# Kernel optimization log

Measured on AMD Instinct MI355X. Metric: run time of the kernel, lower is better.

## Reference

```python
import jax, jax.numpy as jnp
import numpy as np

# dims: B=4 batch, S=512 seq, P=128 input_size, C=64 classes(=hidden_size), K=64 gln layer width, 4 context bits -> 16 contexts
B, S, P, C, K, NBITS = 4, 512, 128, 64, 64, 4
NCTX = 2 ** NBITS
LOGIT_CLIP = 5.0


def setup_inputs() -> dict:
    key = jax.random.key(0)
    ks = jax.random.split(key, 8)
    return {
        "x": jax.random.normal(ks[0], (B, S, P), jnp.float32),
        "hidden": jax.random.normal(ks[1], (B, C), jnp.float32),
        # GLN layer 1: per-class, per-neuron halfspace context hyperplanes and gated weights
        "H1": jax.random.normal(ks[2], (C, K, NBITS, P), jnp.float32),
        "W1": jax.random.normal(ks[3], (C, K, NCTX, P), jnp.float32) / np.sqrt(P),
        # GLN output layer: one neuron per class
        "H2": jax.random.normal(ks[4], (C, NBITS, P), jnp.float32),
        "W2": jax.random.normal(ks[5], (C, NCTX, K), jnp.float32) / np.sqrt(K),
        # fc2: Linear(input_size, hidden_size)
        "fc2_w": jax.random.normal(ks[6], (C, P), jnp.float32) / np.sqrt(P),
        "fc2_b": jnp.zeros((C,), jnp.float32),
    }


def _ctx_index(bits):
    # bits: (..., NBITS) bool -> integer context id in [0, 2^NBITS)
    return (bits * (2 ** jnp.arange(NBITS, dtype=jnp.int32))).sum(-1)


def _gln_predict(x, H1, W1, H2, W2):
    # base predictions: sigmoid(x) -> logit space is x itself (clipped for stability)
    l0 = jnp.clip(x, -LOGIT_CLIP, LOGIT_CLIP)  # (B,S,P)
    # layer 1: halfspace gating then geometric mixing in logit space
    ctx1 = _ctx_index(jnp.einsum('bsp,ckjp->bsckj', x, H1) > 0)          # (B,S,C,K)
    mix1 = jnp.einsum('bsp,ckxp->bsckx', l0, W1)                          # (B,S,C,K,NCTX)
    l1 = jnp.take_along_axis(mix1, ctx1[..., None], axis=-1)[..., 0]      # (B,S,C,K)
    l1 = jnp.clip(l1, -LOGIT_CLIP, LOGIT_CLIP)
    # output layer: one gated neuron per class
    ctx2 = _ctx_index(jnp.einsum('bsp,cjp->bscj', x, H2) > 0)             # (B,S,C)
    mix2 = jnp.einsum('bsck,cxk->bscx', l1, W2)                           # (B,S,C,NCTX)
    l2 = jnp.take_along_axis(mix2, ctx2[..., None], axis=-1)[..., 0]      # (B,S,C)
    return jax.nn.sigmoid(l2)


def reference(x, hidden, H1, W1, H2, W2, fc2_w, fc2_b):
    b = _gln_predict(x, H1, W1, H2, W2)                   # (B,S,C)
    # multihead gating
    sig_alphas = jax.nn.sigmoid(x @ fc2_w.T + fc2_b)      # (B,S,C)
    b = b * sig_alphas

    # sequential roll+add+relu recurrence over seq_len
    def step(h, bt):
        h = jax.nn.relu(bt + jnp.roll(h, 1, axis=-1))
        return h, h

    h_last, outs = jax.lax.scan(step, hidden, jnp.swapaxes(b, 0, 1))  # outs: (S,B,C)
    outputs = jnp.swapaxes(outs, 0, 1)                                # (B,S,C)
    return outputs, h_last
```

## Files before the change

kernel.cpp:

```cpp
#include <hip/hip_runtime.h>
#include <math.h>

#define BB 4
#define SS 512
#define PP 128
#define CC 64
#define KK 64
#define NCTX_ 16
#define TT 64
#define NTILES ((BB*SS)/TT)

typedef __attribute__((ext_vector_type(8))) short bf16x8;
typedef __attribute__((ext_vector_type(4))) float f32x4;
typedef __attribute__((ext_vector_type(16))) float f32x16;

static __device__ __forceinline__ float bf2f(short h) {
    unsigned u = ((unsigned)(unsigned short)h) << 16;
    return __builtin_bit_cast(float, u);
}
static __device__ __forceinline__ short f2bf(float f) {
    unsigned u = __builtin_bit_cast(unsigned, f);
    unsigned r = (u + 0x7fffu + ((u >> 16) & 1u)) >> 16;
    return (short)(unsigned short)r;
}
static __device__ __forceinline__ bf16x8 clampfrag(bf16x8 h) {
    typedef __attribute__((ext_vector_type(4))) unsigned u32x4;
    u32x4 u = __builtin_bit_cast(u32x4, h);
    #pragma unroll
    for (int i = 0; i < 4; ++i) {
        const unsigned w = u[i];
        const unsigned s = w & 0x80008000u;
        unsigned lo = w & 0x7fffu;
        unsigned hi = (w >> 16) & 0x7fffu;
        lo = lo > 0x40a0u ? 0x40a0u : lo;
        hi = hi > 0x40a0u ? 0x40a0u : hi;
        u[i] = s | lo | (hi << 16);
    }
    return __builtin_bit_cast(bf16x8, u);
}

__global__ __launch_bounds__(256) void pack_kernel(
    const float* __restrict__ W1, const float* __restrict__ H1,
    const float* __restrict__ H2, const float* __restrict__ fc2w,
    short* __restrict__ W1h, short* __restrict__ H1h32, short* __restrict__ H1l32,
    short* __restrict__ H2Wh, short* __restrict__ H2Wl)
{
    const int bid  = blockIdx.x;
    const int w    = threadIdx.x >> 6;
    const int lane = threadIdx.x & 63;

    if (bid < CC * KK) {
        const int tile = bid;
        const int q    = w;
        const float4* src = reinterpret_cast<const float4*>(
            W1 + ((size_t)tile * 16 + (lane >> 2)) * PP + q * 32 + (lane & 3) * 8);
        const float4 v0 = src[0], v1 = src[1];
        const float vv[8] = {v0.x, v0.y, v0.z, v0.w, v1.x, v1.y, v1.z, v1.w};
        bf16x8 hh;
        #pragma unroll
        for (int e = 0; e < 8; ++e) hh[e] = f2bf(vv[e]);
        const int lp = (lane & 3) * 16 + (lane >> 2);
        *reinterpret_cast<bf16x8*>(W1h + (((size_t)tile * 4 + q) * 64 + lp) * 8) = hh;
    } else if (bid < CC * KK + 1024) {
        const int gw  = (bid - CC * KK) * 4 + w;
        const int row = (gw >> 3) * 32 + (lane & 31);
        const int col = (gw & 7) * 16 + (lane >> 5) * 8;
        const float4* s = reinterpret_cast<const float4*>(H1 + (size_t)row * PP + col);
        const float4 a = s[0], b = s[1];
        const float vv[8] = {a.x, a.y, a.z, a.w, b.x, b.y, b.z, b.w};
        bf16x8 hh, ll;
        #pragma unroll
        for (int e = 0; e < 8; ++e) {
            const short hv = f2bf(vv[e]);
            hh[e] = hv;
            ll[e] = f2bf(vv[e] - bf2f(hv));
        }
        const size_t o = ((size_t)gw * 64 + lane) * 8;
        *reinterpret_cast<bf16x8*>(H1h32 + o) = hh;
        *reinterpret_cast<bf16x8*>(H1l32 + o) = ll;
    } else {
        const int cidx = bid - (CC * KK + 1024);
        #pragma unroll
        for (int i = 0; i < 2; ++i) {
            const int q8  = w * 2 + i;
            const int row = lane & 31;
            const int col = q8 * 16 + (lane >> 5) * 8;
            float vv[8];
            if (row < 4) {
                const float4* s = reinterpret_cast<const float4*>(
                    H2 + ((size_t)cidx * 4 + row) * PP + col);
                const float4 a = s[0], b = s[1];
                vv[0]=a.x; vv[1]=a.y; vv[2]=a.z; vv[3]=a.w;
                vv[4]=b.x; vv[5]=b.y; vv[6]=b.z; vv[7]=b.w;
            } else if (row == 4) {
                const float4* s = reinterpret_cast<const float4*>(
                    fc2w + (size_t)cidx * PP + col);
                const float4 a = s[0], b = s[1];
                vv[0]=a.x; vv[1]=a.y; vv[2]=a.z; vv[3]=a.w;
                vv[4]=b.x; vv[5]=b.y; vv[6]=b.z; vv[7]=b.w;
            } else {
                #pragma unroll
                for (int e = 0; e < 8; ++e) vv[e] = 0.f;
            }
            bf16x8 hh, ll;
            #pragma unroll
            for (int e = 0; e < 8; ++e) {
                const short hv = f2bf(vv[e]);
                hh[e] = hv;
                ll[e] = f2bf(vv[e] - bf2f(hv));
            }
            const size_t o = (((size_t)cidx * 8 + q8) * 64 + lane) * 8;
            *reinterpret_cast<bf16x8*>(H2Wh + o) = hh;
            *reinterpret_cast<bf16x8*>(H2Wl + o) = ll;
        }
    }
}

__global__ __launch_bounds__(256, 4) void predict_kernel(
    const float* __restrict__ x,
    const short* __restrict__ H1h32,
    const short* __restrict__ H1l32,
    const short* __restrict__ W1h,
    const short* __restrict__ H2Wh,
    const short* __restrict__ H2Wl,
    const float* __restrict__ W2,
    const float* __restrict__ fc2b,
    float* __restrict__ bout)
{
    __shared__ short xuh[2][8][64][8];
    __shared__ short xul[2][8][64][8];
    __shared__ unsigned char ctxb[TT][68];
    __shared__ unsigned char bit2b[TT];
    __shared__ float af[TT];

    const int tid  = threadIdx.x;
    const int lane = tid & 63;
    const int wid  = __builtin_amdgcn_readfirstlane(tid >> 6);
    const int bid  = blockIdx.x;
    const int sw   = ((bid & 7) << 8) | (bid >> 3);
    const int c    = sw >> 5;
    const int tile = sw & (NTILES - 1);
    const int tok0 = tile * TT;

    const int t15 = lane & 15;
    const int g   = lane >> 4;
    const int l31 = lane & 31;
    const int l5  = lane >> 5;
    const f32x4  zero4  = {0.f, 0.f, 0.f, 0.f};
    const f32x16 zero16 = {0.f,0.f,0.f,0.f,0.f,0.f,0.f,0.f,
                           0.f,0.f,0.f,0.f,0.f,0.f,0.f,0.f};

    {
        const int tok = tid >> 2;
        const int qq  = tid & 3;
        const int ct  = tok >> 5;
        const float4* x4 = reinterpret_cast<const float4*>(
            x + (size_t)(tok0 + tok) * PP + qq * 32);
        float v[32];
        #pragma unroll
        for (int i = 0; i < 8; ++i) {
            const float4 t = x4[i];
            v[i*4+0]=t.x; v[i*4+1]=t.y; v[i*4+2]=t.z; v[i*4+3]=t.w;
        }
        #pragma unroll
        for (int gg = 0; gg < 4; ++gg) {
            const int q8 = qq * 2 + (gg >> 1);
            const int lw = (gg & 1) * 32 + (tok & 31);
            bf16x8 hh, ll;
            #pragma unroll
            for (int e = 0; e < 8; ++e) {
                const float f = v[gg*8+e];
                const short hv = f2bf(f);
                hh[e] = hv;
                ll[e] = f2bf(f - bf2f(hv));
            }
            *reinterpret_cast<bf16x8*>(&xuh[ct][q8][lw][0]) = hh;
            *reinterpret_cast<bf16x8*>(&xul[ct][q8][lw][0]) = ll;
        }
    }
    __syncthreads();

    #pragma unroll
    for (int rt = 0; rt < 2; ++rt) {
        f32x16 aA = zero16, aB = zero16;
        const size_t tb = ((size_t)(c * 8 + wid * 2 + rt)) * 8;
        #pragma unroll
        for (int q8 = 0; q8 < 8; ++q8) {
            const size_t fo = ((tb + q8) * 64 + lane) * 8;
            const bf16x8 ah  = *reinterpret_cast<const bf16x8*>(H1h32 + fo);
            const bf16x8 al  = *reinterpret_cast<const bf16x8*>(H1l32 + fo);
            const bf16x8 bh0 = *reinterpret_cast<const bf16x8*>(&xuh[0][q8][lane][0]);
            const bf16x8 bl0 = *reinterpret_cast<const bf16x8*>(&xul[0][q8][lane][0]);
            const bf16x8 bh1 = *reinterpret_cast<const bf16x8*>(&xuh[1][q8][lane][0]);
            const bf16x8 bl1 = *reinterpret_cast<const bf16x8*>(&xul[1][q8][lane][0]);
            aA = __builtin_amdgcn_mfma_f32_32x32x16_bf16(ah, bh0, aA, 0, 0, 0);
            aA = __builtin_amdgcn_mfma_f32_32x32x16_bf16(ah, bl0, aA, 0, 0, 0);
            aA = __builtin_amdgcn_mfma_f32_32x32x16_bf16(al, bh0, aA, 0, 0, 0);
            aB = __builtin_amdgcn_mfma_f32_32x32x16_bf16(ah, bh1, aB, 0, 0, 0);
            aB = __builtin_amdgcn_mfma_f32_32x32x16_bf16(ah, bl1, aB, 0, 0, 0);
            aB = __builtin_amdgcn_mfma_f32_32x32x16_bf16(al, bh1, aB, 0, 0, 0);
        }
        #pragma unroll
        for (int rg = 0; rg < 4; ++rg) {
            const int k = wid * 16 + rt * 8 + 2 * rg + l5;
            const int cvA = (aA[4*rg+0] > 0.f ? 1 : 0) | (aA[4*rg+1] > 0.f ? 2 : 0) |
                            (aA[4*rg+2] > 0.f ? 4 : 0) | (aA[4*rg+3] > 0.f ? 8 : 0);
            const int cvB = (aB[4*rg+0] > 0.f ? 1 : 0) | (aB[4*rg+1] > 0.f ? 2 : 0) |
                            (aB[4*rg+2] > 0.f ? 4 : 0) | (aB[4*rg+3] > 0.f ? 8 : 0);
            ctxb[l31][k]      = (unsigned char)cvA;
            ctxb[32 + l31][k] = (unsigned char)cvB;
        }
    }

    if (wid < 2) {
        f32x16 a2 = zero16;
        #pragma unroll
        for (int q8 = 0; q8 < 8; ++q8) {
            const size_t fo = (((size_t)c * 8 + q8) * 64 + lane) * 8;
            const bf16x8 ah = *reinterpret_cast<const bf16x8*>(H2Wh + fo);
            const bf16x8 al = *reinterpret_cast<const bf16x8*>(H2Wl + fo);
            const bf16x8 bh = *reinterpret_cast<const bf16x8*>(&xuh[wid][q8][lane][0]);
            const bf16x8 bl = *reinterpret_cast<const bf16x8*>(&xul[wid][q8][lane][0]);
            a2 = __builtin_amdgcn_mfma_f32_32x32x16_bf16(ah, bh, a2, 0, 0, 0);
            a2 = __builtin_amdgcn_mfma_f32_32x32x16_bf16(ah, bl, a2, 0, 0, 0);
            a2 = __builtin_amdgcn_mfma_f32_32x32x16_bf16(al, bh, a2, 0, 0, 0);
        }
        const int tok = wid * 32 + l31;
        if (l5 == 0) {
            bit2b[tok] = (unsigned char)((a2[0] > 0.f ? 1 : 0) | (a2[1] > 0.f ? 2 : 0) |
                                         (a2[2] > 0.f ? 4 : 0) | (a2[3] > 0.f ? 8 : 0));
        } else {
            af[tok] = a2[0];
        }
    }
    __syncthreads();

    short* l1s = &xul[0][0][0][0];
    {
        bf16x8 ch[4][4];
        #pragma unroll
        for (int j = 0; j < 4; ++j)
            #pragma unroll
            for (int q = 0; q < 4; ++q) {
                const int q8 = 2 * q + (g >> 1);
                const int lw = (g & 1) * 32 + (j & 1) * 16 + t15;
                ch[j][q] = clampfrag(*reinterpret_cast<const bf16x8*>(&xuh[j >> 1][q8][lw][0]));
            }

        #pragma unroll 4
        for (int k16 = 0; k16 < 16; ++k16) {
            const int k = wid * 16 + k16;
            f32x4 acc[4] = {zero4, zero4, zero4, zero4};
            #pragma unroll
            for (int q = 0; q < 4; ++q) {
                const size_t fo = (((size_t)(c * KK + k) * 4 + q) * 64 + lane) * 8;
                const bf16x8 ah = *reinterpret_cast<const bf16x8*>(W1h + fo);
                #pragma unroll
                for (int j = 0; j < 4; ++j)
                    acc[j] = __builtin_amdgcn_mfma_f32_16x16x32_bf16(ah, ch[j][q], acc[j], 0, 0, 0);
            }
            #pragma unroll
            for (int j = 0; j < 4; ++j) {
                const int tok = j * 16 + t15;
                const int cx  = ctxb[tok][k];
                const int sel = cx & 3;
                const float v = (sel == 0) ? acc[j][0] : (sel == 1) ? acc[j][1] :
                                (sel == 2) ? acc[j][2] : acc[j][3];
                if (g == (cx >> 2))
                    l1s[tok * 68 + k] = f2bf(fminf(fmaxf(v, -5.f), 5.f));
            }
        }
    }
    __syncthreads();

    {
        const int tok = tid >> 2;
        const int qt  = tid & 3;
        const int ctx2 = bit2b[tok];
        const float4* w2p = reinterpret_cast<const float4*>(
            W2 + ((size_t)c * NCTX_ + ctx2) * KK + qt * 16);
        float s = 0.f;
        #pragma unroll
        for (int i4 = 0; i4 < 4; ++i4) {
            const float4 w = w2p[i4];
            const int kb = tok * 68 + qt * 16 + i4 * 4;
            s = fmaf(w.x, bf2f(l1s[kb + 0]),
                fmaf(w.y, bf2f(l1s[kb + 1]),
                fmaf(w.z, bf2f(l1s[kb + 2]),
                fmaf(w.w, bf2f(l1s[kb + 3]), s))));
        }
        s += __shfl_xor(s, 1, 64);
        s += __shfl_xor(s, 2, 64);
        if (qt == 0) {
            const float alpha = af[tok] + fc2b[c];
            const float bv = (1.f / (1.f + expf(-s))) * (1.f / (1.f + expf(-alpha)));
            bout[(size_t)(tok0 + tok) * CC + c] = bv;
        }
    }
}

__global__ __launch_bounds__(256, 4) void predict_fb_kernel(
    const float* __restrict__ x,
    const float* __restrict__ H1,
    const float* __restrict__ W1b,
    const float* __restrict__ H2,
    const float* __restrict__ W2,
    const float* __restrict__ fc2w,
    const float* __restrict__ fc2b,
    float* __restrict__ bout)
{
    __shared__ float xs[PP][TT + 1];
    __shared__ float bitss[4][TT];
    __shared__ float apart[4][TT];
    __shared__ float l2part[4][TT];

    const int tid  = threadIdx.x;
    const int lane = tid & 63;
    const int wid  = __builtin_amdgcn_readfirstlane(tid >> 6);
    const int bid  = blockIdx.x;
    const int sw   = ((bid & 7) << 8) | (bid >> 3);
    const int c    = sw >> 5;
    const int tile = sw & (NTILES - 1);
    const int tok0 = tile * TT;

    {
        const float4* xg = reinterpret_cast<const float4*>(x + (size_t)tok0 * PP);
        #pragma unroll
        for (int it = 0; it < (TT * PP / 4) / 256; ++it) {
            const int i = it * 256 + tid;
            const float4 v = xg[i];
            const int t = i >> 5;
            const int p = (i & 31) << 2;
            xs[p + 0][t] = v.x; xs[p + 1][t] = v.y;
            xs[p + 2][t] = v.z; xs[p + 3][t] = v.w;
        }
    }
    __syncthreads();

    int ctxreg[16];
    {
        const float4* H1c4 = reinterpret_cast<const float4*>(H1 + (size_t)c * KK * 4 * PP);
        #pragma unroll
        for (int gg = 0; gg < 8; ++gg) {
            const int k = wid * 16 + gg * 2;
            const float4* h4 = H1c4 + (size_t)k * 4 * 32;
            float acc[8] = {0.f, 0.f, 0.f, 0.f, 0.f, 0.f, 0.f, 0.f};
            #pragma unroll 2
            for (int p4 = 0; p4 < 32; ++p4) {
                const float x0 = xs[4 * p4 + 0][lane];
                const float x1 = xs[4 * p4 + 1][lane];
                const float x2 = xs[4 * p4 + 2][lane];
                const float x3 = xs[4 * p4 + 3][lane];
                #pragma unroll
                for (int r = 0; r < 8; ++r) {
                    const float4 w = h4[r * 32 + p4];
                    acc[r] = fmaf(w.w, x3, fmaf(w.z, x2, fmaf(w.y, x1, fmaf(w.x, x0, acc[r]))));
                }
            }
            ctxreg[gg * 2]     = (acc[0] > 0.f ? 1 : 0) | (acc[1] > 0.f ? 2 : 0) |
                                 (acc[2] > 0.f ? 4 : 0) | (acc[3] > 0.f ? 8 : 0);
            ctxreg[gg * 2 + 1] = (acc[4] > 0.f ? 1 : 0) | (acc[5] > 0.f ? 2 : 0) |
                                 (acc[6] > 0.f ? 4 : 0) | (acc[7] > 0.f ? 8 : 0);
        }
    }
    {
        const float4* h2 = reinterpret_cast<const float4*>(H2 + ((size_t)c * 4 + wid) * PP);
        float d = 0.f;
        #pragma unroll 8
        for (int p4 = 0; p4 < 32; ++p4) {
            const float4 w = h2[p4];
            d = fmaf(w.w, xs[4 * p4 + 3][lane], fmaf(w.z, xs[4 * p4 + 2][lane],
                fmaf(w.y, xs[4 * p4 + 1][lane], fmaf(w.x, xs[4 * p4 + 0][lane], d))));
        }
        bitss[wid][lane] = (d > 0.f) ? 1.f : 0.f;
        const float4* fw = reinterpret_cast<const float4*>(fc2w + (size_t)c * PP) + wid * 8;
        float ap = 0.f;
        #pragma unroll
        for (int p4 = 0; p4 < 8; ++p4) {
            const float4 w = fw[p4];
            const int p = wid * 32 + 4 * p4;
            ap = fmaf(w.w, xs[p + 3][lane], fmaf(w.z, xs[p + 2][lane],
                 fmaf(w.y, xs[p + 1][lane], fmaf(w.x, xs[p + 0][lane], ap))));
        }
        apart[wid][lane] = ap;
    }
    __syncthreads();

    float l1v[16];
    {
        const float4* W1c4 = reinterpret_cast<const float4*>(W1b) +
                             (size_t)(c * KK + wid * 16) * 512;
        #pragma unroll
        for (int gg = 0; gg < 2; ++gg) {
            float s[8] = {0.f, 0.f, 0.f, 0.f, 0.f, 0.f, 0.f, 0.f};
            const float4* wp[8];
            #pragma unroll
            for (int jj = 0; jj < 8; ++jj) {
                const int kk = gg * 8 + jj;
                wp[jj] = W1c4 + (size_t)kk * 512 + (size_t)ctxreg[kk] * 32;
            }
            #pragma unroll 2
            for (int p4 = 0; p4 < 32; ++p4) {
                const float x0 = fminf(fmaxf(xs[4 * p4 + 0][lane], -5.f), 5.f);
                const float x1 = fminf(fmaxf(xs[4 * p4 + 1][lane], -5.f), 5.f);
                const float x2 = fminf(fmaxf(xs[4 * p4 + 2][lane], -5.f), 5.f);
                const float x3 = fminf(fmaxf(xs[4 * p4 + 3][lane], -5.f), 5.f);
                #pragma unroll
                for (int jj = 0; jj < 8; ++jj) {
                    const float4 wv = wp[jj][p4];
                    s[jj] = fmaf(wv.w, x3, fmaf(wv.z, x2, fmaf(wv.y, x1, fmaf(wv.x, x0, s[jj]))));
                }
            }
            #pragma unroll
            for (int jj = 0; jj < 8; ++jj)
                l1v[gg * 8 + jj] = fminf(fmaxf(s[jj], -5.f), 5.f);
        }
    }
    {
        const int ctx2 = (bitss[0][lane] > 0.5f ? 1 : 0) | (bitss[1][lane] > 0.5f ? 2 : 0) |
                         (bitss[2][lane] > 0.5f ? 4 : 0) | (bitss[3][lane] > 0.5f ? 8 : 0);
        const float* w2 = W2 + ((size_t)c * NCTX_ + ctx2) * KK + wid * 16;
        float lp = 0.f;
        #pragma unroll
        for (int jj = 0; jj < 16; ++jj) lp = fmaf(w2[jj], l1v[jj], lp);
        l2part[wid][lane] = lp;
    }
    __syncthreads();
    if (wid == 0) {
        const int t = lane;
        const float l2 = (l2part[0][t] + l2part[1][t]) + (l2part[2][t] + l2part[3][t]);
        const float alpha = apart[0][t] + apart[1][t] + apart[2][t] + apart[3][t] + fc2b[c];
        const float bv = (1.f / (1.f + expf(-l2))) * (1.f / (1.f + expf(-alpha)));
        bout[(size_t)(tok0 + t) * CC + c] = bv;
    }
}

__global__ __launch_bounds__(64) void scan_kernel(const float* __restrict__ hidden,
                                                  float* __restrict__ out)
{
    const int b    = blockIdx.x;
    const int lane = threadIdx.x;
    float* row = out + (size_t)b * SS * CC;
    const float hprev = hidden[b * CC + ((lane + 63) & 63)];

    float nb[64];
    #pragma unroll
    for (int j = 0; j < 64; ++j) nb[j] = row[j * CC + ((lane + j) & 63)];
    float acc = fmaxf(nb[0] + hprev, 0.f);
    row[lane] = acc;
    #pragma unroll
    for (int j = 1; j < 64; ++j) {
        acc += nb[j];
        row[j * CC + ((lane + j) & 63)] = acc;
    }
    for (int c0 = 64; c0 < SS; c0 += 64) {
        #pragma unroll
        for (int j = 0; j < 64; ++j)
            nb[j] = row[(c0 + j) * CC + ((lane + c0 + j) & 63)];
        #pragma unroll
        for (int j = 0; j < 64; ++j) {
            acc += nb[j];
            row[(c0 + j) * CC + ((lane + c0 + j) & 63)] = acc;
        }
    }
    out[(size_t)BB * SS * CC + b * CC + ((lane + 63) & 63)] = acc;
}

extern "C" void kernel_launch(void* const* d_in, const int* in_sizes, int n_in,
                              void* d_out, int out_size, void* d_ws, size_t ws_size,
                              hipStream_t stream) {
    const float* x      = (const float*)d_in[0];
    const float* hidden = (const float*)d_in[1];
    const float* H1     = (const float*)d_in[2];
    const float* W1     = (const float*)d_in[3];
    const float* H2     = (const float*)d_in[4];
    const float* W2     = (const float*)d_in[5];
    const float* fc2w   = (const float*)d_in[6];
    const float* fc2b   = (const float*)d_in[7];
    float* out = (float*)d_out;

    const size_t MB = 1024 * 1024;

    if (ws_size >= 25 * MB) {
        short* W1hp  = (short*)d_ws;
        short* H1hp  = (short*)((char*)d_ws + 16 * MB);
        short* H1lp  = (short*)((char*)d_ws + 20 * MB);
        short* H2Whp = (short*)((char*)d_ws + 24 * MB);
        short* H2Wlp = (short*)((char*)d_ws + 24 * MB + 512 * 1024);
        pack_kernel<<<dim3(CC * KK + 1024 + CC), 256, 0, stream>>>(
            W1, H1, H2, fc2w, W1hp, H1hp, H1lp, H2Whp, H2Wlp);
        predict_kernel<<<dim3(CC * NTILES), 256, 0, stream>>>(
            x, H1hp, H1lp, W1hp, H2Whp, H2Wlp, W2, fc2b, out);
    } else {
        predict_fb_kernel<<<dim3(CC * NTILES), 256, 0, stream>>>(
            x, H1, W1, H2, W2, fc2w, fc2b, out);
    }
    scan_kernel<<<dim3(BB), 64, 0, stream>>>(hidden, out);
}
```

Before: 104.4 us.

## Switch GLN layer-1 mixing to 32x32x16 MFMA with repacked W1 fragments

Repacks W1 into 32-row A fragments that cover two neurons × 16 contexts each, and computes layer-1 mixing with 32x32x16 bf16 MFMAs over two 32-token halves instead of 16x16x32 MFMAs per neuron. The context-selected value is pulled from the larger accumulator with an 8-way select. The clamp of the x fragments is moved into a separate shared-memory pass before the loop, so it is no longer applied per register fragment. The goal is fewer MFMA issues and fewer A-fragment loads per output. The cost is higher accumulator register pressure and an extra barrier.

```diff
diff --git a/kernel.cpp b/kernel.cpp
--- a/kernel.cpp
+++ b/kernel.cpp
@@ -38,6 +38,13 @@
     }
     return __builtin_bit_cast(bf16x8, u);
 }
+template <int BASE>
+static __device__ __forceinline__ float sel8(const f32x16& a, int sel) {
+    return sel == 0 ? a[BASE + 0] : sel == 1 ? a[BASE + 1] :
+           sel == 2 ? a[BASE + 2] : sel == 3 ? a[BASE + 3] :
+           sel == 4 ? a[BASE + 4] : sel == 5 ? a[BASE + 5] :
+           sel == 6 ? a[BASE + 6] : a[BASE + 7];
+}
 
 __global__ __launch_bounds__(256) void pack_kernel(
     const float* __restrict__ W1, const float* __restrict__ H1,
@@ -49,20 +56,25 @@
     const int w    = threadIdx.x >> 6;
     const int lane = threadIdx.x & 63;
 
-    if (bid < CC * KK) {
-        const int tile = bid;
-        const int q    = w;
-        const float4* src = reinterpret_cast<const float4*>(
-            W1 + ((size_t)tile * 16 + (lane >> 2)) * PP + q * 32 + (lane & 3) * 8);
-        const float4 v0 = src[0], v1 = src[1];
-        const float vv[8] = {v0.x, v0.y, v0.z, v0.w, v1.x, v1.y, v1.z, v1.w};
+    if (bid < 4096) {
+        const int gw  = bid * 4 + w;
+        const int q8  = gw & 7;
+        const int m   = (gw >> 3) & 31;
+        const int cc  = gw >> 8;
+        const int r   = lane & 31;
+        const int k   = 2 * m + (r >> 4);
+        const int ctx = r & 15;
+        const int col = q8 * 16 + (lane >> 5) * 8;
+        const float4* s = reinterpret_cast<const float4*>(
+            W1 + (((size_t)(cc * KK + k) * NCTX_ + ctx) * PP + col));
+        const float4 a = s[0], b = s[1];
+        const float vv[8] = {a.x, a.y, a.z, a.w, b.x, b.y, b.z, b.w};
         bf16x8 hh;
         #pragma unroll
         for (int e = 0; e < 8; ++e) hh[e] = f2bf(vv[e]);
-        const int lp = (lane & 3) * 16 + (lane >> 2);
-        *reinterpret_cast<bf16x8*>(W1h + (((size_t)tile * 4 + q) * 64 + lp) * 8) = hh;
-    } else if (bid < CC * KK + 1024) {
-        const int gw  = (bid - CC * KK) * 4 + w;
+        *reinterpret_cast<bf16x8*>(W1h + ((size_t)gw * 64 + lane) * 8) = hh;
+    } else if (bid < 4096 + 1024) {
+        const int gw  = (bid - 4096) * 4 + w;
         const int row = (gw >> 3) * 32 + (lane & 31);
         const int col = (gw & 7) * 16 + (lane >> 5) * 8;
         const float4* s = reinterpret_cast<const float4*>(H1 + (size_t)row * PP + col);
@@ -79,7 +91,7 @@
         *reinterpret_cast<bf16x8*>(H1h32 + o) = hh;
         *reinterpret_cast<bf16x8*>(H1l32 + o) = ll;
     } else {
-        const int cidx = bid - (CC * KK + 1024);
+        const int cidx = bid - (4096 + 1024);
         #pragma unroll
         for (int i = 0; i < 2; ++i) {
             const int q8  = w * 2 + i;
@@ -142,11 +154,8 @@
     const int tile = sw & (NTILES - 1);
     const int tok0 = tile * TT;
 
-    const int t15 = lane & 15;
-    const int g   = lane >> 4;
     const int l31 = lane & 31;
     const int l5  = lane >> 5;
-    const f32x4  zero4  = {0.f, 0.f, 0.f, 0.f};
     const f32x16 zero16 = {0.f,0.f,0.f,0.f,0.f,0.f,0.f,0.f,
                            0.f,0.f,0.f,0.f,0.f,0.f,0.f,0.f};
 
@@ -235,39 +244,46 @@
     }
     __syncthreads();
 
+    {
+        bf16x8* xp = reinterpret_cast<bf16x8*>(&xuh[0][0][0][0]);
+        #pragma unroll
+        for (int i = 0; i < 8; ++i) {
+            const int idx = i * 256 + tid;
+            xp[idx] = clampfrag(xp[idx]);
+        }
+    }
+    __syncthreads();
+
     short* l1s = &xul[0][0][0][0];
     {
-        bf16x8 ch[4][4];
-        #pragma unroll
-        for (int j = 0; j < 4; ++j)
+        #pragma unroll 2
+        for (int m = 0; m < 8; ++m) {
+            const int pr = wid * 8 + m;
+            const int k0 = 2 * pr, k1 = 2 * pr + 1;
+            f32x16 a0 = zero16, a1 = zero16;
             #pragma unroll
-            for (int q = 0; q < 4; ++q) {
-                const int q8 = 2 * q + (g >> 1);
-                const int lw = (g & 1) * 32 + (j & 1) * 16 + t15;
-                ch[j][q] = clampfrag(*reinterpret_cast<const bf16x8*>(&xuh[j >> 1][q8][lw][0]));
-            }
-
-        #pragma unroll 4
-        for (int k16 = 0; k16 < 16; ++k16) {
-            const int k = wid * 16 + k16;
-            f32x4 acc[4] = {zero4, zero4, zero4, zero4};
+            for (int q8 = 0; q8 < 8; ++q8) {
+                const size_t fo = (((size_t)(c * 32 + pr) * 8 + q8) * 64 + lane) * 8;
+                const bf16x8 ah = *reinterpret_cast<const bf16x8*>(W1h + fo);
+                const bf16x8 b0 = *reinterpret_cast<const bf16x8*>(&xuh[0][q8][lane][0]);
+                const bf16x8 b1 = *reinterpret_cast<const bf16x8*>(&xuh[1][q8][lane][0]);
+                a0 = __builtin_amdgcn_mfma_f32_32x32x16_bf16(ah, b0, a0, 0, 0, 0);
+                a1 = __builtin_amdgcn_mfma_f32_32x32x16_bf16(ah, b1, a1, 0, 0, 0);
+            }
             #pragma unroll
-            for (int q = 0; q < 4; ++q) {
-                const size_t fo = (((size_t)(c * KK + k) * 4 + q) * 64 + lane) * 8;
-                const bf16x8 ah = *reinterpret_cast<const bf16x8*>(W1h + fo);
-                #pragma unroll
-                for (int j = 0; j < 4; ++j)
-                    acc[j] = __builtin_amdgcn_mfma_f32_16x16x32_bf16(ah, ch[j][q], acc[j], 0, 0, 0);
-            }
-            #pragma unroll
-            for (int j = 0; j < 4; ++j) {
-                const int tok = j * 16 + t15;
-                const int cx  = ctxb[tok][k];
-                const int sel = cx & 3;
-                const float v = (sel == 0) ? acc[j][0] : (sel == 1) ? acc[j][1] :
-                                (sel == 2) ? acc[j][2] : acc[j][3];
-                if (g == (cx >> 2))
-                    l1s[tok * 68 + k] = f2bf(fminf(fmaxf(v, -5.f), 5.f));
+            for (int ct = 0; ct < 2; ++ct) {
+                const f32x16& av = ct ? a1 : a0;
+                const int tok = ct * 32 + l31;
+                const int cx0 = ctxb[tok][k0];
+                const int cx1 = ctxb[tok][k1];
+                if (l5 == ((cx0 >> 2) & 1)) {
+                    const float v = sel8<0>(av, (cx0 & 3) + ((cx0 >> 3) << 2));
+                    l1s[tok * 68 + k0] = f2bf(fminf(fmaxf(v, -5.f), 5.f));
+                }
+                if (l5 == ((cx1 >> 2) & 1)) {
+                    const float v = sel8<8>(av, (cx1 & 3) + ((cx1 >> 3) << 2));
+                    l1s[tok * 68 + k1] = f2bf(fminf(fmaxf(v, -5.f), 5.f));
+                }
             }
         }
     }
@@ -487,7 +503,7 @@
         short* H1lp  = (short*)((char*)d_ws + 20 * MB);
         short* H2Whp = (short*)((char*)d_ws + 24 * MB);
         short* H2Wlp = (short*)((char*)d_ws + 24 * MB + 512 * 1024);
-        pack_kernel<<<dim3(CC * KK + 1024 + CC), 256, 0, stream>>>(
+        pack_kernel<<<dim3(4096 + 1024 + CC), 256, 0, stream>>>(
             W1, H1, H2, fc2w, W1hp, H1hp, H1lp, H2Whp, H2Wlp);
         predict_kernel<<<dim3(CC * NTILES), 256, 0, stream>>>(
             x, H1hp, H1lp, W1hp, H2Whp, H2Wlp, W2, fc2b, out);
```

Measured after the change: 107.7 us. 3.2% more time.

## Drop low-order bf16 split of x in gating matmuls and remove a barrier

Applied to the files above, without the earlier changes.

The kernel no longer keeps a low bf16 residual of x in shared memory. The H1 and H2 halfspace dot products therefore use 2 MFMAs per step instead of 3. The freed shared memory becomes a dedicated l1 buffer, which lets the block barrier between context computation and the W1 mixing phase go, since each wave only reads context entries it wrote itself. Launch bounds are raised to 5 blocks per CU for more occupancy. The cost is reduced precision in the sign tests that pick contexts, so tokens near a hyperplane may select a different context.

```diff
diff --git a/kernel.cpp b/kernel.cpp
--- a/kernel.cpp
+++ b/kernel.cpp
@@ -116,7 +116,7 @@
     }
 }
 
-__global__ __launch_bounds__(256, 4) void predict_kernel(
+__global__ __launch_bounds__(256, 5) void predict_kernel(
     const float* __restrict__ x,
     const short* __restrict__ H1h32,
     const short* __restrict__ H1l32,
@@ -128,7 +128,7 @@
     float* __restrict__ bout)
 {
     __shared__ short xuh[2][8][64][8];
-    __shared__ short xul[2][8][64][8];
+    __shared__ short l1s[TT][68];
     __shared__ unsigned char ctxb[TT][68];
     __shared__ unsigned char bit2b[TT];
     __shared__ float af[TT];
@@ -166,16 +166,10 @@
         for (int gg = 0; gg < 4; ++gg) {
             const int q8 = qq * 2 + (gg >> 1);
             const int lw = (gg & 1) * 32 + (tok & 31);
-            bf16x8 hh, ll;
-            #pragma unroll
-            for (int e = 0; e < 8; ++e) {
-                const float f = v[gg*8+e];
-                const short hv = f2bf(f);
-                hh[e] = hv;
-                ll[e] = f2bf(f - bf2f(hv));
-            }
+            bf16x8 hh;
+            #pragma unroll
+            for (int e = 0; e < 8; ++e) hh[e] = f2bf(v[gg*8+e]);
             *reinterpret_cast<bf16x8*>(&xuh[ct][q8][lw][0]) = hh;
-            *reinterpret_cast<bf16x8*>(&xul[ct][q8][lw][0]) = ll;
         }
     }
     __syncthreads();
@@ -190,14 +184,10 @@
             const bf16x8 ah  = *reinterpret_cast<const bf16x8*>(H1h32 + fo);
             const bf16x8 al  = *reinterpret_cast<const bf16x8*>(H1l32 + fo);
             const bf16x8 bh0 = *reinterpret_cast<const bf16x8*>(&xuh[0][q8][lane][0]);
-            const bf16x8 bl0 = *reinterpret_cast<const bf16x8*>(&xul[0][q8][lane][0]);
             const bf16x8 bh1 = *reinterpret_cast<const bf16x8*>(&xuh[1][q8][lane][0]);
-            const bf16x8 bl1 = *reinterpret_cast<const bf16x8*>(&xul[1][q8][lane][0]);
             aA = __builtin_amdgcn_mfma_f32_32x32x16_bf16(ah, bh0, aA, 0, 0, 0);
-            aA = __builtin_amdgcn_mfma_f32_32x32x16_bf16(ah, bl0, aA, 0, 0, 0);
             aA = __builtin_amdgcn_mfma_f32_32x32x16_bf16(al, bh0, aA, 0, 0, 0);
             aB = __builtin_amdgcn_mfma_f32_32x32x16_bf16(ah, bh1, aB, 0, 0, 0);
-            aB = __builtin_amdgcn_mfma_f32_32x32x16_bf16(ah, bl1, aB, 0, 0, 0);
             aB = __builtin_amdgcn_mfma_f32_32x32x16_bf16(al, bh1, aB, 0, 0, 0);
         }
         #pragma unroll
@@ -220,9 +210,7 @@
             const bf16x8 ah = *reinterpret_cast<const bf16x8*>(H2Wh + fo);
             const bf16x8 al = *reinterpret_cast<const bf16x8*>(H2Wl + fo);
             const bf16x8 bh = *reinterpret_cast<const bf16x8*>(&xuh[wid][q8][lane][0]);
-            const bf16x8 bl = *reinterpret_cast<const bf16x8*>(&xul[wid][q8][lane][0]);
             a2 = __builtin_amdgcn_mfma_f32_32x32x16_bf16(ah, bh, a2, 0, 0, 0);
-            a2 = __builtin_amdgcn_mfma_f32_32x32x16_bf16(ah, bl, a2, 0, 0, 0);
             a2 = __builtin_amdgcn_mfma_f32_32x32x16_bf16(al, bh, a2, 0, 0, 0);
         }
         const int tok = wid * 32 + l31;
@@ -233,9 +221,7 @@
             af[tok] = a2[0];
         }
     }
-    __syncthreads();
-
-    short* l1s = &xul[0][0][0][0];
+
     {
         bf16x8 ch[4][4];
         #pragma unroll
@@ -267,7 +253,7 @@
                 const float v = (sel == 0) ? acc[j][0] : (sel == 1) ? acc[j][1] :
                                 (sel == 2) ? acc[j][2] : acc[j][3];
                 if (g == (cx >> 2))
-                    l1s[tok * 68 + k] = f2bf(fminf(fmaxf(v, -5.f), 5.f));
+                    l1s[tok][k] = f2bf(fminf(fmaxf(v, -5.f), 5.f));
             }
         }
     }
@@ -283,11 +269,11 @@
         #pragma unroll
         for (int i4 = 0; i4 < 4; ++i4) {
             const float4 w = w2p[i4];
-            const int kb = tok * 68 + qt * 16 + i4 * 4;
-            s = fmaf(w.x, bf2f(l1s[kb + 0]),
-                fmaf(w.y, bf2f(l1s[kb + 1]),
-                fmaf(w.z, bf2f(l1s[kb + 2]),
-                fmaf(w.w, bf2f(l1s[kb + 3]), s))));
+            const int kb = qt * 16 + i4 * 4;
+            s = fmaf(w.x, bf2f(l1s[tok][kb + 0]),
+                fmaf(w.y, bf2f(l1s[tok][kb + 1]),
+                fmaf(w.z, bf2f(l1s[tok][kb + 2]),
+                fmaf(w.w, bf2f(l1s[tok][kb + 3]), s))));
         }
         s += __shfl_xor(s, 1, 64);
         s += __shfl_xor(s, 2, 64);
```

After: 115.5 us. 10.6% more time.
